# Kernel optimization log

Measured on AMD Instinct MI355X. Metric: run time of the kernel, lower is better.

Reference implementation:

```python
import jax, jax.numpy as jnp
import numpy as np
import math

N, S, R = 1, 128, 256
CM, CZ, C, MSA_H, PAIR_H, CTM, FF = 256, 128, 32, 8, 4, 128, 4
SCALE = 1.0 / math.sqrt(C)


def _ln(x, w, b):
    m = jnp.mean(x, -1, keepdims=True)
    v = jnp.var(x, -1, keepdims=True)
    return (x - m) / jnp.sqrt(v + 1e-5) * w + b


def _gated_attn(x, gate_w, qkv_w, out_w, head, bias=None):
    # x: [n, s, r, cin]; attention over r within each (n, s, head)
    n, s, r, _ = x.shape
    gate = jax.nn.sigmoid(x @ gate_w).reshape(n, s, r, head, C)
    qkv = (x @ qkv_w).reshape(n, s, r, 3, head, C)
    q, k, v = qkv[..., 0, :, :], qkv[..., 1, :, :], qkv[..., 2, :, :]
    sim = jax.nn.softmax(jnp.einsum('nsqhc,nskhc->nshqk', q, k) * SCALE, axis=-1)
    if bias is not None:
        sim = sim + bias  # NOTE: source adds bias AFTER softmax; kept faithful
    att = jnp.einsum('nshqk,nskhc->nsqhc', sim, v) * gate
    return att.reshape(n, s, r, head * C) @ out_w


def _tri_mul(x, n1w, n1b, n2w, n2b, p1, p2, p3, p4, p5, p6, incoming):
    xn = _ln(x, n1w, n1b)
    a = jax.nn.sigmoid(xn @ p1) * (xn @ p2)
    b = jax.nn.sigmoid(xn @ p3) * (xn @ p4)
    if incoming:
        p = jnp.einsum('nrsk,nrtk->nstk', a, b)
        g = jnp.swapaxes(jax.nn.sigmoid(xn @ p6), 1, 2)
    else:
        p = jnp.einsum('nsrk,ntrk->nstk', a, b)
        g = jax.nn.sigmoid(xn @ p6)
    return (_ln(p, n2w, n2b) @ p5) * g


def setup_inputs() -> dict:
    keys = iter(jax.random.split(jax.random.key(0), 80))

    def rn(shape, scale=0.02):
        return jax.random.normal(next(keys), shape, dtype=jnp.float32) * scale

    ones = lambda n: jnp.ones((n,), jnp.float32)
    zeros = lambda n: jnp.zeros((n,), jnp.float32)
    d = dict(
        msa_repr=rn((N, S, R, CM), 1.0),
        pair_repr=rn((N, R, R, CZ), 1.0),
        row_norm_m_w=ones(CM), row_norm_m_b=zeros(CM),
        row_norm_z_w=ones(CZ), row_norm_z_b=zeros(CZ),
        row_gate=rn((CM, MSA_H * C)), row_qkv=rn((CM, 3 * MSA_H * C)),
        row_out=rn((MSA_H * C, CM)), row_bias=rn((CZ, MSA_H)),
        col_norm_w=ones(CM), col_norm_b=zeros(CM),
        col_gate=rn((CM, MSA_H * C)), col_qkv=rn((CM, 3 * MSA_H * C)),
        col_out=rn((MSA_H * C, CM)),
        mt_norm_w=ones(CM), mt_norm_b=zeros(CM),
        mt_p1=rn((CM, FF * CM)), mt_p2=rn((FF * CM, CM)),
        outer_norm_w=ones(CM), outer_norm_b=zeros(CM),
        outer_p1=rn((CM, C)), outer_p2=rn((CM, C)), outer_out=rn((C * C, CZ)),
        tmo_n1_w=ones(CZ), tmo_n1_b=zeros(CZ), tmo_n2_w=ones(CTM), tmo_n2_b=zeros(CTM),
        tmo_p1=rn((CZ, CTM)), tmo_p2=rn((CZ, CTM)), tmo_p3=rn((CZ, CTM)), tmo_p4=rn((CZ, CTM)),
        tmo_p5=rn((CTM, CZ)), tmo_p6=rn((CZ, CZ)),
        tmi_n1_w=ones(CZ), tmi_n1_b=zeros(CZ), tmi_n2_w=ones(CTM), tmi_n2_b=zeros(CTM),
        tmi_p1=rn((CZ, CTM)), tmi_p2=rn((CZ, CTM)), tmi_p3=rn((CZ, CTM)), tmi_p4=rn((CZ, CTM)),
        tmi_p5=rn((CTM, CZ)), tmi_p6=rn((CZ, CZ)),
        tas_norm_w=ones(CZ), tas_norm_b=zeros(CZ),
        tas_gate=rn((CZ, PAIR_H * C)), tas_qkv=rn((CZ, 3 * PAIR_H * C)),
        tas_out=rn((PAIR_H * C, CZ)), tas_bias=rn((CZ, PAIR_H)),
        tae_norm_w=ones(CZ), tae_norm_b=zeros(CZ),
        tae_gate=rn((CZ, PAIR_H * C)), tae_qkv=rn((CZ, 3 * PAIR_H * C)),
        tae_out=rn((PAIR_H * C, CZ)), tae_bias=rn((CZ, PAIR_H)),
        pt_norm_w=ones(CZ), pt_norm_b=zeros(CZ),
        pt_p1=rn((CZ, FF * CZ)), pt_p2=rn((FF * CZ, CZ)),
    )
    return d


def reference(msa_repr, pair_repr, row_norm_m_w, row_norm_m_b, row_norm_z_w, row_norm_z_b, row_gate, row_qkv, row_out, row_bias, col_norm_w, col_norm_b, col_gate, col_qkv, col_out, mt_norm_w, mt_norm_b, mt_p1, mt_p2, outer_norm_w, outer_norm_b, outer_p1, outer_p2, outer_out, tmo_n1_w, tmo_n1_b, tmo_n2_w, tmo_n2_b, tmo_p1, tmo_p2, tmo_p3, tmo_p4, tmo_p5, tmo_p6, tmi_n1_w, tmi_n1_b, tmi_n2_w, tmi_n2_b, tmi_p1, tmi_p2, tmi_p3, tmi_p4, tmi_p5, tmi_p6, tas_norm_w, tas_norm_b, tas_gate, tas_qkv, tas_out, tas_bias, tae_norm_w, tae_norm_b, tae_gate, tae_qkv, tae_out, tae_bias, pt_norm_w, pt_norm_b, pt_p1, pt_p2):
    msa, pair = msa_repr, pair_repr
    # 1. MSA row attention with pair bias
    xm = _ln(msa, row_norm_m_w, row_norm_m_b)
    xz = _ln(pair, row_norm_z_w, row_norm_z_b)
    bias = jnp.transpose(xz @ row_bias, (0, 3, 1, 2))[:, None]  # [N,1,H,R,R]
    msa = msa + _gated_attn(xm, row_gate, row_qkv, row_out, MSA_H, bias)
    # 2. MSA column attention
    xm = _ln(msa, col_norm_w, col_norm_b)
    msa = msa + jnp.swapaxes(_gated_attn(jnp.swapaxes(xm, 1, 2), col_gate, col_qkv, col_out, MSA_H), 1, 2)
    # 3. MSA transition
    xm = _ln(msa, mt_norm_w, mt_norm_b)
    msa = msa + jax.nn.relu(xm @ mt_p1) @ mt_p2
    # 4. outer product mean (no division in source; sum over s)
    xm = _ln(msa, outer_norm_w, outer_norm_b)
    a = jnp.swapaxes(xm @ outer_p1, 1, 2)  # [n,r,s,c]
    b = jnp.swapaxes(xm @ outer_p2, 1, 2)  # [n,t,s,c]
    outer = jnp.einsum('nrsc,ntse->nrtce', a, b).reshape(a.shape[0], a.shape[1], b.shape[1], C * C)
    pair = pair + outer @ outer_out
    # 5/6. triangle multiplicative updates (outgoing then incoming)
    pair = pair + _tri_mul(pair, tmo_n1_w, tmo_n1_b, tmo_n2_w, tmo_n2_b, tmo_p1, tmo_p2, tmo_p3, tmo_p4, tmo_p5, tmo_p6, False)
    pair = pair + _tri_mul(pair, tmi_n1_w, tmi_n1_b, tmi_n2_w, tmi_n2_b, tmi_p1, tmi_p2, tmi_p3, tmi_p4, tmi_p5, tmi_p6, True)
    # 7. triangle attention (node start)
    xz = _ln(pair, tas_norm_w, tas_norm_b)
    bias = jnp.transpose(xz @ tas_bias, (0, 1, 3, 2))[:, :, :, None, :]  # [N,S,H,1,R]
    pair = pair + _gated_attn(xz, tas_gate, tas_qkv, tas_out, PAIR_H, bias)
    # 8. triangle attention (node end): transpose residue axes
    xz = jnp.swapaxes(_ln(pair, tae_norm_w, tae_norm_b), 1, 2)
    bias = jnp.transpose(xz @ tae_bias, (0, 1, 3, 2))[:, :, :, None, :]
    pair = pair + jnp.swapaxes(_gated_attn(xz, tae_gate, tae_qkv, tae_out, PAIR_H, bias), 1, 2)
    # 9. pair transition
    xz = _ln(pair, pt_norm_w, pt_norm_b)
    pair = pair + jax.nn.relu(xz @ pt_p1) @ pt_p2
    return msa, pair
```

## Files before the change

kernel.cpp:

```cpp
#include <hip/hip_runtime.h>
#include <hip/hip_bf16.h>
#include <stdint.h>

typedef __hip_bfloat16 bf16;
typedef __attribute__((ext_vector_type(4))) int   i32x4;
typedef __attribute__((ext_vector_type(4))) float f32x4;


__device__ __forceinline__ float toF(float x){ return x; }
__device__ __forceinline__ float toF(bf16 x){ return __bfloat162float(x); }
__device__ __forceinline__ bf16  toB(float x){ return __float2bfloat16(x); }

__device__ __forceinline__ void gload16(const bf16* g, bf16* l){
    __builtin_amdgcn_global_load_lds((const __attribute__((address_space(1))) void*)g,
                                     (__attribute__((address_space(3))) void*)l, 16, 0, 0);
}

__global__ void cvt_w_k(const void* __restrict__ in, bf16* __restrict__ out, int n,
                        const uint32_t* __restrict__ probe){
    bool isbf = (probe[0] == 0x3F803F80u);
    int i = blockIdx.x*256 + threadIdx.x;
    if (i < n) out[i] = isbf ? ((const bf16*)in)[i] : toB(((const float*)in)[i]);
}
__global__ void cvt_wT_k(const void* __restrict__ in, bf16* __restrict__ out, int K, int N,
                         const uint32_t* __restrict__ probe){
    bool isbf = (probe[0] == 0x3F803F80u);
    int i = blockIdx.x*256 + threadIdx.x;
    if (i < K*N){
        float v = isbf ? toF(((const bf16*)in)[i]) : ((const float*)in)[i];
        int k = i / N, n = i - k*N;
        out[(size_t)n*K + k] = toB(v);
    }
}
__global__ void in2f_k(const void* __restrict__ in, float* __restrict__ out, int n,
                       const uint32_t* __restrict__ probe){
    bool isbf = (probe[0] == 0x3F803F80u);
    int i = blockIdx.x*256 + threadIdx.x;
    if (i < n) out[i] = isbf ? toF(((const bf16*)in)[i]) : ((const float*)in)[i];
}

template<typename T>
__global__ void ln_k(const T* __restrict__ x, const bf16* __restrict__ w, const bf16* __restrict__ b,
                     bf16* __restrict__ out, int D){
    int row = blockIdx.x, c = threadIdx.x;
    float v = toF(x[(size_t)row*D + c]);
    float s1 = v, s2 = v*v;
    #pragma unroll
    for (int o=32;o>0;o>>=1){ s1 += __shfl_down(s1,o); s2 += __shfl_down(s2,o); }
    __shared__ float r1[4], r2[4];
    int lane = c & 63, wid = c >> 6;
    if (lane==0){ r1[wid]=s1; r2[wid]=s2; }
    __syncthreads();
    int nw = blockDim.x >> 6;
    float m=0.f, q=0.f;
    for (int i=0;i<nw;i++){ m+=r1[i]; q+=r2[i]; }
    m /= (float)D; q = q/(float)D - m*m;
    float inv = rsqrtf(q + 1e-5f);
    out[(size_t)row*D + c] = toB((v-m)*inv*toF(w[c]) + toF(b[c]));
}

template<int MODE, int HN>
__global__ __launch_bounds__(256) void bproj_k(const bf16* __restrict__ xz, const bf16* __restrict__ Wb,
                                               float* __restrict__ outb){
    __shared__ float WbS[128*HN];
    const int i = blockIdx.x, t = threadIdx.x;
    for (int idx = t; idx < 128*HN; idx += 256) WbS[idx] = toF(Wb[idx]);
    __syncthreads();
    const bf16* row = xz + ((size_t)i*256 + t)*128;
    float d[HN] = {};
    #pragma unroll 4
    for (int c8 = 0; c8 < 16; ++c8){
        uint4 v = *(const uint4*)(row + c8*8);
        bf16 tmp[8]; *(uint4*)tmp = v;
        #pragma unroll
        for (int u=0;u<8;u++){
            float x = toF(tmp[u]);
            #pragma unroll
            for (int h=0;h<HN;h++) d[h] += x * WbS[(c8*8+u)*HN + h];
        }
    }
    #pragma unroll
    for (int h=0;h<HN;h++){
        size_t idx = (MODE==0) ? ((size_t)h*65536 + (size_t)i*256 + t)
                   : (MODE==1) ? ((size_t)(i*HN+h)*256 + t)
                               : ((size_t)(t*HN+h)*256 + i);
        outb[idx] = d[h];
    }
}

template<int ACT, int MUL, int RES>
__global__ __launch_bounds__(256) void mgemm_k(const bf16* __restrict__ A, const bf16* __restrict__ Bt,
                                               bf16* __restrict__ C, float* __restrict__ Res,
                                               const bf16* __restrict__ Mul,
                                               int M, int N, int K, int lda, int ldbt, int ldc,
                                               int res_off, int gtrans){
    __shared__ alignas(16) bf16 As[128*32];
    __shared__ alignas(16) bf16 Bs[128*32];
    const int tid  = threadIdx.x;
    const int m0   = blockIdx.y << 7, n0 = blockIdx.x << 7;
    const int lane = tid & 63, w = tid >> 6;
    const int wr   = (w >> 1) << 6, wc = (w & 1) << 6;
    const int fr   = lane & 15, fq = lane >> 4;
    const int sr = tid >> 2, sc = (tid & 3) << 3;
    const bf16* ga = A  + (size_t)(m0 + sr)*lda  + sc;
    const bf16* gb = Bt + (size_t)(n0 + sr)*ldbt + sc;
    bf16* la = As + tid*8;
    bf16* lb = Bs + tid*8;
    const size_t gaS = (size_t)64*lda, gbS = (size_t)64*ldbt;

    f32x4 acc[4][4] = {};
    for (int k0=0; k0<K; k0+=32){
        gload16(ga, la);        gload16(ga + gaS, la + 2048);
        gload16(gb, lb);        gload16(gb + gbS, lb + 2048);
        ga += 32; gb += 32;
        __syncthreads();
        i32x4 af[4], bv[4];
        #pragma unroll
        for (int i=0;i<4;i++) af[i] = *(const i32x4*)(As + ((wr + i*16 + fr) << 5) + (fq << 3));
        #pragma unroll
        for (int j=0;j<4;j++) bv[j] = *(const i32x4*)(Bs + ((wc + j*16 + fr) << 5) + (fq << 3));
        #pragma unroll
        for (int i=0;i<4;i++)
            #pragma unroll
            for (int j=0;j<4;j++)
                asm("v_mfma_f32_16x16x32_bf16 %0, %1, %2, %0"
                    : "+v"(acc[i][j]) : "v"(af[i]), "v"(bv[j]));
        __syncthreads();
    }
    #pragma unroll
    for (int i=0;i<4;i++){
        const int mB = m0 + wr + i*16 + (fq << 2);
        #pragma unroll
        for (int j=0;j<4;j++){
            const int n = n0 + wc + j*16 + fr;
            #pragma unroll
            for (int r=0;r<4;r++){
                int m = mB + r;
                float x = acc[i][j][r];
                if (ACT==1) x = 1.f/(1.f + __expf(-x));
                else if (ACT==2) x = fmaxf(x, 0.f);
                if (MUL){
                    int mr = gtrans ? (((m & 255) << 8) | (m >> 8)) : m;
                    x *= toF(Mul[(size_t)mr*N + n]);
                }
                if (RES) Res[(size_t)(m + res_off)*N + n] += x;
                else     C[(size_t)m*ldc + n] = toB(x);
            }
        }
    }
}

template<int ACT, int MUL, int RES, int GATE>
__global__ __launch_bounds__(256) void sgemm_k(const bf16* __restrict__ A,
        const bf16* __restrict__ Bt1, const bf16* __restrict__ Bt2,
        bf16* __restrict__ C, float* __restrict__ Res, const bf16* __restrict__ Mul,
        int M, int lda, int ldbt, int ldc, int ldmul, int res_off, int gtrans){
    __shared__ alignas(16) bf16 Bs1[128*128];
    __shared__ alignas(16) bf16 Bs2[GATE ? 128*128 : 16];
    const int tid = threadIdx.x;
    for (int idx = tid; idx < 2048; idx += 256){
        int n = idx >> 4, cc = idx & 15;
        int sc = (cc ^ (n & 15)) << 3;
        *(uint4*)(Bs1 + n*128 + sc) = *(const uint4*)(Bt1 + (size_t)n*ldbt + (cc<<3));
        if (GATE)
            *(uint4*)(Bs2 + n*128 + sc) = *(const uint4*)(Bt2 + (size_t)n*ldbt + (cc<<3));
    }
    __syncthreads();
    const int lane = tid & 63, w = tid >> 6;
    const int fr = lane & 15, fq = lane >> 4;
    const int mb = blockIdx.x*128 + w*32;
    f32x4 acc[2][8] = {};
    f32x4 acc2[2][8] = {};
    #pragma unroll
    for (int k0=0;k0<4;k0++){
        i32x4 af[2];
        #pragma unroll
        for (int i=0;i<2;i++)
            af[i] = *(const i32x4*)(A + (size_t)(mb + i*16 + fr)*lda + k0*32 + fq*8);
        const int co = ((k0*4 + fq) ^ fr) << 3;
        #pragma unroll
        for (int j=0;j<8;j++){
            i32x4 bf1 = *(const i32x4*)(Bs1 + (j*16+fr)*128 + co);
            #pragma unroll
            for (int i=0;i<2;i++)
                asm("v_mfma_f32_16x16x32_bf16 %0, %1, %2, %0"
                    : "+v"(acc[i][j]) : "v"(af[i]), "v"(bf1));
            if (GATE){
                i32x4 bf2 = *(const i32x4*)(Bs2 + (j*16+fr)*128 + co);
                #pragma unroll
                for (int i=0;i<2;i++)
                    asm("v_mfma_f32_16x16x32_bf16 %0, %1, %2, %0"
                        : "+v"(acc2[i][j]) : "v"(af[i]), "v"(bf2));
            }
        }
    }
    #pragma unroll
    for (int i=0;i<2;i++){
        #pragma unroll
        for (int j=0;j<8;j++){
            const int n = j*16 + fr;
            #pragma unroll
            for (int r=0;r<4;r++){
                int m = mb + i*16 + (fq<<2) + r;
                float x = acc[i][j][r];
                if (GATE) x = acc2[i][j][r] / (1.f + __expf(-x));
                else if (ACT==1) x = 1.f/(1.f + __expf(-x));
                else if (ACT==2) x = fmaxf(x, 0.f);
                if (MUL){
                    int mr = gtrans ? (((m & 255) << 8) | (m >> 8)) : m;
                    x *= toF(Mul[(size_t)mr*ldmul + n]);
                }
                if (RES) Res[(size_t)(m + res_off)*128 + n] += x;
                else     C[(size_t)m*ldc + n] = toB(x);
            }
        }
    }
}

__global__ __launch_bounds__(256) void btrimul_k(const bf16* __restrict__ aT, const bf16* __restrict__ bT,
                                                 bf16* __restrict__ pT){
    __shared__ alignas(16) bf16 As[128*32];
    __shared__ alignas(16) bf16 Bs[128*32];
    const int tid  = threadIdx.x;
    const int m0   = blockIdx.y << 7, n0 = blockIdx.x << 7;
    const size_t zb = (size_t)blockIdx.z << 16;
    const int lane = tid & 63, w = tid >> 6;
    const int wr   = (w >> 1) << 6, wc = (w & 1) << 6;
    const int fr   = lane & 15, fq = lane >> 4;
    const int sr = tid >> 2, sc = (tid & 3) << 3;
    const bf16* ga = aT + zb + (size_t)(m0 + sr)*256 + sc;
    const bf16* gb = bT + zb + (size_t)(n0 + sr)*256 + sc;
    bf16* la = As + tid*8;
    bf16* lb = Bs + tid*8;
    const size_t gS = (size_t)64*256;

    f32x4 acc[4][4] = {};
    for (int k0=0; k0<256; k0+=32){
        gload16(ga, la);        gload16(ga + gS, la + 2048);
        gload16(gb, lb);        gload16(gb + gS, lb + 2048);
        ga += 32; gb += 32;
        __syncthreads();
        i32x4 af[4], bv[4];
        #pragma unroll
        for (int i=0;i<4;i++) af[i] = *(const i32x4*)(As + ((wr + i*16 + fr) << 5) + (fq << 3));
        #pragma unroll
        for (int j=0;j<4;j++) bv[j] = *(const i32x4*)(Bs + ((wc + j*16 + fr) << 5) + (fq << 3));
        #pragma unroll
        for (int i=0;i<4;i++)
            #pragma unroll
            for (int j=0;j<4;j++)
                asm("v_mfma_f32_16x16x32_bf16 %0, %1, %2, %0"
                    : "+v"(acc[i][j]) : "v"(af[i]), "v"(bv[j]));
        __syncthreads();
    }
    #pragma unroll
    for (int i=0;i<4;i++){
        const int mB = m0 + wr + i*16 + (fq << 2);
        #pragma unroll
        for (int j=0;j<4;j++){
            const int n = n0 + wc + j*16 + fr;
            #pragma unroll
            for (int r=0;r<4;r++)
                pT[zb + (size_t)(mB + r)*256 + n] = toB(acc[i][j][r]);
        }
    }
}

__global__ __launch_bounds__(256) void rc2k_k(const bf16* __restrict__ in, bf16* __restrict__ out, int swap){
    __shared__ uint16_t T[128][137];
    const int tt = blockIdx.x, tid = threadIdx.x;
    size_t base_pp, out_off; int ppstride;
    if (!swap){ base_pp = (size_t)tt*128;                  ppstride = 1;   out_off = (size_t)tt*128; }
    else      { int J = tt>>1, I0 = (tt&1)*128;
                base_pp = (size_t)I0*256 + J;              ppstride = 256; out_off = (size_t)J*256 + I0; }
    for (int it=0; it<8; ++it){
        int idx = tid + it*256;
        int r = idx >> 4, c8 = (idx & 15) << 3;
        uint4 v = *(const uint4*)(in + (base_pp + (size_t)r*ppstride)*128 + c8);
        uint16_t tmp[8]; *(uint4*)tmp = v;
        #pragma unroll
        for (int t=0;t<8;t++) T[r][c8+t] = tmp[t];
    }
    __syncthreads();
    for (int it=0; it<8; ++it){
        int idx = tid + it*256;
        int k = idx >> 4, r8 = (idx & 15) << 3;
        uint16_t tmp[8];
        #pragma unroll
        for (int t=0;t<8;t++) tmp[t] = T[r8+t][k];
        *(uint4*)(out + (size_t)k*65536 + out_off + r8) = *(uint4*)tmp;
    }
}
__global__ __launch_bounds__(256) void k2rc_k(const bf16* __restrict__ in, bf16* __restrict__ out){
    __shared__ uint16_t T[128][137];
    const int tt = blockIdx.x, tid = threadIdx.x;
    const size_t a0 = (size_t)tt*128;
    for (int it=0; it<8; ++it){
        int idx = tid + it*256;
        int k = idx >> 4, r8 = (idx & 15) << 3;
        uint4 v = *(const uint4*)(in + (size_t)k*65536 + a0 + r8);
        uint16_t tmp[8]; *(uint4*)tmp = v;
        #pragma unroll
        for (int t=0;t<8;t++) T[r8+t][k] = tmp[t];
    }
    __syncthreads();
    for (int it=0; it<8; ++it){
        int idx = tid + it*256;
        int r = idx >> 4, c8 = (idx & 15) << 3;
        uint16_t tmp[8];
        #pragma unroll
        for (int t=0;t<8;t++) tmp[t] = T[r][c8+t];
        *(uint4*)(out + (a0 + r)*128 + c8) = *(uint4*)tmp;
    }
}

template<int ACT, int MUL, int RES>
__global__ __launch_bounds__(256) void gemm_k(const bf16* __restrict__ A, const bf16* __restrict__ Bw,
                                              bf16* __restrict__ C, float* __restrict__ Res,
                                              const bf16* __restrict__ Mul,
                                              int M, int N, int K, int ldb, int res_off, int gtrans){
    __shared__ float As[64][33];
    __shared__ float Bs[32][65];
    int tid = threadIdx.x;
    int m0 = blockIdx.y*64, n0 = blockIdx.x*64;
    int tx = tid & 15, ty = tid >> 4;
    float acc[4][4] = {};
    for (int k0=0; k0<K; k0+=32){
        for (int i=tid; i<64*32; i+=256){
            int r = i>>5, cc = i&31;
            As[r][cc] = toF(A[(size_t)(m0+r)*K + k0 + cc]);
        }
        for (int i=tid; i<32*64; i+=256){
            int r = i>>6, cc = i&63; int col = n0+cc;
            Bs[r][cc] = (col < N) ? toF(Bw[(size_t)(k0+r)*ldb + col]) : 0.f;
        }
        __syncthreads();
        #pragma unroll 8
        for (int k=0;k<32;k++){
            float a4[4], b4[4];
            #pragma unroll
            for (int i=0;i<4;i++) a4[i] = As[ty*4+i][k];
            #pragma unroll
            for (int j=0;j<4;j++) b4[j] = Bs[k][tx*4+j];
            #pragma unroll
            for (int i=0;i<4;i++)
                #pragma unroll
                for (int j=0;j<4;j++) acc[i][j] += a4[i]*b4[j];
        }
        __syncthreads();
    }
    #pragma unroll
    for (int i=0;i<4;i++){
        int m = m0 + ty*4 + i;
        #pragma unroll
        for (int j=0;j<4;j++){
            int n = n0 + tx*4 + j;
            if (n >= N) continue;
            float x = acc[i][j];
            if (ACT==1) x = 1.f/(1.f + __expf(-x));
            else if (ACT==2) x = fmaxf(x, 0.f);
            if (MUL){
                int mr = gtrans ? (((m & 255) << 8) | (m >> 8)) : m;
                x *= toF(Mul[(size_t)mr*N + n]);
            }
            if (RES) Res[(size_t)(m + res_off)*N + n] += x;
            else     C[(size_t)m*N + n] = toB(x);
        }
    }
}

template<int BIAS, int L>
__global__ __launch_bounds__(256) void attn4_k(bf16* __restrict__ QO,
                                               const bf16* __restrict__ Kp, const bf16* __restrict__ Vp,
                                               const float* __restrict__ bias,
                                               int H, int GN, int sO, int sL){
    constexpr int MW  = L/4;
    constexpr int IFR = MW/16;
    constexpr int KC  = 32;
    constexpr int NCH = L/KC;
    constexpr int VP  = L + 8;
    __shared__ alignas(16) bf16 K_lds[L*40];
    __shared__ alignas(16) bf16 VT_lds[32*VP];
    __shared__ alignas(16) bf16 P_lds[L*40];
    __shared__ float red[8*32 + 32];
    const int o = blockIdx.y, h = blockIdx.x, tid = threadIdx.x;
    const int lane = tid & 63, w = tid >> 6;
    const int fr = lane & 15, fq = lane >> 4;

    for (int idx = tid; idx < L*4; idx += 256){
        int l = idx >> 2, c8 = (idx & 3) << 3;
        size_t p = (size_t)(o*sO + l*sL)*GN + h*32 + c8;
        *(uint4*)(K_lds + l*40 + c8) = *(const uint4*)(Kp + p);
        uint4 vv = *(const uint4*)(Vp + p);
        bf16 tmp[8]; *(uint4*)tmp = vv;
        #pragma unroll
        for (int t=0;t<8;t++) VT_lds[(c8+t)*VP + l] = tmp[t];
    }
    __syncthreads();

    float* ObS = red + 256;
    if (BIAS == 2){
        int c = tid & 31, g = tid >> 5;
        const float* bp = bias + (size_t)(o*H + h)*256;
        float p = 0.f;
        for (int k = g*(L/8); k < (g+1)*(L/8); ++k)
            p += bp[k] * toF(VT_lds[c*VP + k]);
        red[g*32 + c] = p;
        __syncthreads();
        if (tid < 32){
            float s = 0.f;
            #pragma unroll
            for (int g2=0; g2<8; ++g2) s += red[g2*32 + tid];
            ObS[tid] = s;
        }
        __syncthreads();
    }

    i32x4 qf[IFR];
    #pragma unroll
    for (int i=0;i<IFR;i++){
        int q = w*MW + i*16 + fr;
        qf[i] = *(const i32x4*)(QO + (size_t)(o*sO + q*sL)*GN + h*32 + fq*8);
    }
    bf16* Pw = P_lds + w*MW*40;
    f32x4 accO[IFR][2] = {};
    f32x4 accB[IFR][2] = {};
    float lsum[IFR][4] = {};

    for (int ch=0; ch<NCH; ++ch){
        const int k0 = ch*KC;
        f32x4 sa[IFR][2] = {};
        i32x4 kf[2];
        #pragma unroll
        for (int j=0;j<2;j++) kf[j] = *(const i32x4*)(K_lds + (k0 + j*16 + fr)*40 + fq*8);
        #pragma unroll
        for (int i=0;i<IFR;i++)
            #pragma unroll
            for (int j=0;j<2;j++)
                asm("v_mfma_f32_16x16x32_bf16 %0, %1, %2, %0"
                    : "+v"(sa[i][j]) : "v"(qf[i]), "v"(kf[j]));
        #pragma unroll
        for (int i=0;i<IFR;i++)
            #pragma unroll
            for (int j=0;j<2;j++)
                #pragma unroll
                for (int r=0;r<4;r++){
                    float e = __expf(sa[i][j][r] * 0.17677669529663687f);
                    lsum[i][r] += e;
                    Pw[(i*16 + fq*4 + r)*40 + j*16 + fr] = toB(e);
                }
        i32x4 vf[2];
        #pragma unroll
        for (int j=0;j<2;j++) vf[j] = *(const i32x4*)(VT_lds + (j*16 + fr)*VP + k0 + fq*8);
        #pragma unroll
        for (int i=0;i<IFR;i++){
            i32x4 pa = *(const i32x4*)(Pw + (i*16 + fr)*40 + fq*8);
            #pragma unroll
            for (int j=0;j<2;j++)
                asm("v_mfma_f32_16x16x32_bf16 %0, %1, %2, %0"
                    : "+v"(accO[i][j]) : "v"(pa), "v"(vf[j]));
        }
        if (BIAS == 1){
            #pragma unroll
            for (int it=0; it<32; ++it){
                int q = it*2 + (lane>>5), kk = lane&31;
                Pw[q*40 + kk] = toB(bias[(size_t)h*65536 + (size_t)(w*MW + q)*256 + k0 + kk]);
            }
            #pragma unroll
            for (int i=0;i<IFR;i++){
                i32x4 pa = *(const i32x4*)(Pw + (i*16 + fr)*40 + fq*8);
                #pragma unroll
                for (int j=0;j<2;j++)
                    asm("v_mfma_f32_16x16x32_bf16 %0, %1, %2, %0"
                        : "+v"(accB[i][j]) : "v"(pa), "v"(vf[j]));
            }
        }
    }
    #pragma unroll
    for (int i=0;i<IFR;i++)
        #pragma unroll
        for (int r=0;r<4;r++){
            float s = lsum[i][r];
            s += __shfl_xor(s, 1); s += __shfl_xor(s, 2);
            s += __shfl_xor(s, 4); s += __shfl_xor(s, 8);
            lsum[i][r] = 1.f / s;
        }
    #pragma unroll
    for (int i=0;i<IFR;i++)
        #pragma unroll
        for (int j=0;j<2;j++)
            #pragma unroll
            for (int r=0;r<4;r++){
                int q = w*MW + i*16 + fq*4 + r;
                int c = j*16 + fr;
                float v = accO[i][j][r]*lsum[i][r];
                if (BIAS==1) v += accB[i][j][r];
                if (BIAS==2) v += ObS[c];
                QO[(size_t)(o*sO + q*sL)*GN + h*32 + c] = toB(v);
            }
}

__global__ void mulsig2_k(bf16* __restrict__ a, int n){
    int i = blockIdx.x*256 + threadIdx.x;
    if (i < n){
        int m = i >> 8, c = i & 255;
        size_t o = (size_t)m*768 + c;
        float sg = 1.f/(1.f + __expf(-toF(a[o + 256])));
        a[o] = toB(toF(a[o]) * sg);
    }
}

__global__ __launch_bounds__(256) void outer_k(const bf16* __restrict__ ap, const bf16* __restrict__ bp,
                                               bf16* __restrict__ outc, int r0){
    int t = blockIdx.x, rl = blockIdx.y, r = r0 + rl;
    __shared__ float As[128*32], Bs[128*32];
    for (int idx=threadIdx.x; idx<128*32; idx+=256){
        int s = idx>>5, c = idx&31;
        As[idx] = toF(ap[((size_t)s*256 + r)*32 + c]);
        Bs[idx] = toF(bp[((size_t)s*256 + t)*32 + c]);
    }
    __syncthreads();
    int ce0 = threadIdx.x*4;
    int c = ce0 >> 5, e0 = ce0 & 31;
    float acc[4] = {0.f,0.f,0.f,0.f};
    for (int s=0;s<128;s++){
        float av = As[s*32 + c];
        #pragma unroll
        for (int j=0;j<4;j++) acc[j] += av*Bs[s*32 + e0 + j];
    }
    size_t row = (size_t)rl*256 + t;
    #pragma unroll
    for (int j=0;j<4;j++) outc[row*1024 + ce0 + j] = toB(acc[j]);
}

static bool tshape(int i, int& K, int& N){
    switch(i){
        case 6: case 8: case 12: case 14: K=256; N=256;  return true;
        case 7: case 13:                  K=256; N=768;  return true;
        case 17:                          K=256; N=1024; return true;
        case 18:                          K=1024;N=256;  return true;
        case 23:                          K=1024;N=128;  return true;
        case 47: case 53:                 K=128; N=384;  return true;
        case 58:                          K=128; N=512;  return true;
        case 59:                          K=512; N=128;  return true;
        default:
            if ((i>=28&&i<=33)||(i>=38&&i<=43)||i==46||i==48||i==52||i==54){ K=128; N=128; return true; }
            return false;
    }
}

extern "C" void kernel_launch(void* const* d_in, const int* in_sizes, int n_in,
                              void* d_out, int out_size, void* d_ws, size_t ws_size,
                              hipStream_t stream){
    (void)n_in; (void)out_size; (void)ws_size;
    const int MSA_N  = 128*256*256;
    const int PAIR_N = 256*256*128;
    const uint32_t* probe = (const uint32_t*)d_in[2];

    char*  w     = (char*)d_ws;
    bf16*  wsts  = (bf16*)(w);
    float* biasF = (float*)(w + 4194304);
    bf16*  lnb   = (bf16*)(w + 6291456);
    bf16*  bufA  = (bf16*)(w + 23068672);
    bf16*  bufB  = (bf16*)(w + 39845888);
    bf16*  bufC  = (bf16*)(w + 56623104);

    float* msaF  = (float*)d_out;
    float* pairF = msaF + MSA_N;

    size_t woff[64]; { size_t acc = 0;
        for (int i=2;i<60;i++){ woff[i] = acc; acc += ((size_t)in_sizes[i] + 63) & ~(size_t)63; } }
    #define W(i) (wsts + woff[i])
    for (int i=2;i<60;i++){
        int tk, tn;
        if (tshape(i, tk, tn))
            cvt_wT_k<<<(in_sizes[i]+255)/256,256,0,stream>>>(d_in[i], W(i), tk, tn, probe);
        else
            cvt_w_k<<<(in_sizes[i]+255)/256,256,0,stream>>>(d_in[i], W(i), in_sizes[i], probe);
    }

    in2f_k<<<32768,256,0,stream>>>(d_in[0], msaF,  MSA_N,  probe);
    in2f_k<<<32768,256,0,stream>>>(d_in[1], pairF, PAIR_N, probe);

    ln_k<float><<<32768,256,0,stream>>>(msaF, W(2), W(3), lnb, 256);
    ln_k<float><<<65536,128,0,stream>>>(pairF, W(4), W(5), bufC, 128);
    bproj_k<0,8><<<256,256,0,stream>>>(bufC, W(9), biasF);
    mgemm_k<0,0,0><<<dim3(6,256),256,0,stream>>>(lnb, W(7), bufA, nullptr, nullptr,
                                                 32768,768,256, 256,256,768, 0,0);
    attn4_k<1,256><<<dim3(8,128),256,0,stream>>>(bufA, bufA+256, bufA+512, biasF, 8, 768, 256, 1);
    mgemm_k<0,0,0><<<dim3(2,256),256,0,stream>>>(lnb, W(6), bufA+256, nullptr, nullptr,
                                                 32768,256,256, 256,256,768, 0,0);
    mulsig2_k<<<32768,256,0,stream>>>(bufA, MSA_N);
    mgemm_k<0,0,1><<<dim3(2,256),256,0,stream>>>(bufA, W(8), nullptr, msaF, nullptr,
                                                 32768,256,256, 768,256,256, 0,0);

    ln_k<float><<<32768,256,0,stream>>>(msaF, W(10), W(11), lnb, 256);
    mgemm_k<0,0,0><<<dim3(6,256),256,0,stream>>>(lnb, W(13), bufA, nullptr, nullptr,
                                                 32768,768,256, 256,256,768, 0,0);
    attn4_k<0,128><<<dim3(8,256),256,0,stream>>>(bufA, bufA+256, bufA+512, nullptr, 8, 768, 1, 256);
    mgemm_k<0,0,0><<<dim3(2,256),256,0,stream>>>(lnb, W(12), bufA+256, nullptr, nullptr,
                                                 32768,256,256, 256,256,768, 0,0);
    mulsig2_k<<<32768,256,0,stream>>>(bufA, MSA_N);
    mgemm_k<0,0,1><<<dim3(2,256),256,0,stream>>>(bufA, W(14), nullptr, msaF, nullptr,
                                                 32768,256,256, 768,256,256, 0,0);

    ln_k<float><<<32768,256,0,stream>>>(msaF, W(15), W(16), lnb, 256);
    for (int ch=0; ch<4; ++ch){
        mgemm_k<2,0,0><<<dim3(2,256),256,0,stream>>>(lnb, W(17)+ch*65536, bufA, nullptr, nullptr,
                                                     32768,256,256, 256,256,256, 0,0);
        mgemm_k<0,0,1><<<dim3(2,256),256,0,stream>>>(bufA, W(18)+ch*256, nullptr, msaF, nullptr,
                                                     32768,256,256, 256,1024,256, 0,0);
    }

    ln_k<float><<<32768,256,0,stream>>>(msaF, W(19), W(20), lnb, 256);
    gemm_k<0,0,0><<<dim3(1,512),256,0,stream>>>(lnb, W(21), bufA, nullptr, nullptr, 32768,32,256, 32, 0,0);
    gemm_k<0,0,0><<<dim3(1,512),256,0,stream>>>(lnb, W(22), bufB, nullptr, nullptr, 32768,32,256, 32, 0,0);
    for (int ch=0; ch<8; ++ch){
        outer_k<<<dim3(256,32),256,0,stream>>>(bufA, bufB, lnb, ch*32);
        mgemm_k<0,0,1><<<dim3(1,64),256,0,stream>>>(lnb, W(23), nullptr, pairF, nullptr,
                                                    8192,128,1024, 1024,1024,128, ch*8192,0);
    }

    for (int tm=0; tm<2; ++tm){
        int o = tm ? 34 : 24;
        int inc = tm;
        ln_k<float><<<65536,128,0,stream>>>(pairF, W(o+0), W(o+1), lnb, 128);
        sgemm_k<0,0,0,1><<<512,256,0,stream>>>(lnb, W(o+4), W(o+5), bufA, nullptr, nullptr,
                                               65536, 128,128,128,0, 0,0);
        sgemm_k<0,0,0,1><<<512,256,0,stream>>>(lnb, W(o+6), W(o+7), bufB, nullptr, nullptr,
                                               65536, 128,128,128,0, 0,0);
        rc2k_k<<<512,256,0,stream>>>(bufA, bufC, inc);
        rc2k_k<<<512,256,0,stream>>>(bufB, bufA, inc);
        btrimul_k<<<dim3(2,2,128),256,0,stream>>>(bufC, bufA, bufB);
        k2rc_k<<<512,256,0,stream>>>(bufB, bufC);
        ln_k<bf16><<<65536,128,0,stream>>>(bufC, W(o+2), W(o+3), bufC, 128);
        sgemm_k<1,0,0,0><<<512,256,0,stream>>>(lnb, W(o+9), nullptr, bufA, nullptr, nullptr,
                                               65536, 128,128,128,0, 0,0);
        sgemm_k<0,1,1,0><<<512,256,0,stream>>>(bufC, W(o+8), nullptr, nullptr, pairF, bufA,
                                               65536, 128,128,0,128, 0, inc);
    }

    ln_k<float><<<65536,128,0,stream>>>(pairF, W(44), W(45), lnb, 128);
    bproj_k<1,4><<<256,256,0,stream>>>(lnb, W(49), biasF);
    mgemm_k<0,0,0><<<dim3(3,512),256,0,stream>>>(lnb, W(47), bufA, nullptr, nullptr,
                                                 65536,384,128, 128,128,384, 0,0);
    attn4_k<2,256><<<dim3(4,256),256,0,stream>>>(bufA, bufA+128, bufA+256, biasF, 4, 384, 256, 1);
    sgemm_k<1,1,0,0><<<512,256,0,stream>>>(lnb, W(46), nullptr, bufA+128, nullptr, bufA,
                                           65536, 128,128,384,384, 0,0);
    sgemm_k<0,0,1,0><<<512,256,0,stream>>>(bufA+128, W(48), nullptr, nullptr, pairF, nullptr,
                                           65536, 384,128,0,0, 0,0);
    ln_k<float><<<65536,128,0,stream>>>(pairF, W(50), W(51), lnb, 128);
    bproj_k<2,4><<<256,256,0,stream>>>(lnb, W(55), biasF);
    mgemm_k<0,0,0><<<dim3(3,512),256,0,stream>>>(lnb, W(53), bufA, nullptr, nullptr,
                                                 65536,384,128, 128,128,384, 0,0);
    attn4_k<2,256><<<dim3(4,256),256,0,stream>>>(bufA, bufA+128, bufA+256, biasF, 4, 384, 1, 256);
    sgemm_k<1,1,0,0><<<512,256,0,stream>>>(lnb, W(52), nullptr, bufA+128, nullptr, bufA,
                                           65536, 128,128,384,384, 0,0);
    sgemm_k<0,0,1,0><<<512,256,0,stream>>>(bufA+128, W(54), nullptr, nullptr, pairF, nullptr,
                                           65536, 384,128,0,0, 0,0);

    ln_k<float><<<65536,128,0,stream>>>(pairF, W(56), W(57), lnb, 128);
    for (int ch=0; ch<4; ++ch){
        sgemm_k<2,0,0,0><<<512,256,0,stream>>>(lnb, W(58)+ch*16384, nullptr, bufA, nullptr, nullptr,
                                               65536, 128,128,128,0, 0,0);
        sgemm_k<0,0,1,0><<<512,256,0,stream>>>(bufA, W(59)+ch*128, nullptr, nullptr, pairF, nullptr,
                                               65536, 128,512,0,0, 0,0);
    }
}
```

Baseline: 2.557 ms.

## Batch weight conversions into one launch and read attention K fragments directly from global

The 58 per-weight conversion kernel launches become a single launch that indexes each weight by blockIdx.y and uses grid-stride loops, which cuts launch overhead. Separately, the attention kernel stops staging K in LDS and loads each MFMA K fragment straight from global memory. This saves LDS space and a copy, but the K loads become strided global reads inside the inner loop, which adds latency.

```diff
diff --git a/kernel.cpp b/kernel.cpp
--- a/kernel.cpp
+++ b/kernel.cpp
@@ -16,20 +16,24 @@
                                      (__attribute__((address_space(3))) void*)l, 16, 0, 0);
 }
 
-__global__ void cvt_w_k(const void* __restrict__ in, bf16* __restrict__ out, int n,
-                        const uint32_t* __restrict__ probe){
+#define NW_IN 58
+struct WStage {
+    const void* src[NW_IN];
+    int off[NW_IN];
+    int K[NW_IN], N[NW_IN];
+};
+__global__ __launch_bounds__(256) void cvt_all_k(WStage t, bf16* __restrict__ base,
+                                                 const uint32_t* __restrict__ probe){
     bool isbf = (probe[0] == 0x3F803F80u);
-    int i = blockIdx.x*256 + threadIdx.x;
-    if (i < n) out[i] = isbf ? ((const bf16*)in)[i] : toB(((const float*)in)[i]);
-}
-__global__ void cvt_wT_k(const void* __restrict__ in, bf16* __restrict__ out, int K, int N,
-                         const uint32_t* __restrict__ probe){
-    bool isbf = (probe[0] == 0x3F803F80u);
-    int i = blockIdx.x*256 + threadIdx.x;
-    if (i < K*N){
+    const int wi = blockIdx.y;
+    const void* in = t.src[wi];
+    bf16* out = base + t.off[wi];
+    const int K = t.K[wi], N = t.N[wi];
+    const int total = K ? K*N : N;
+    for (int i = blockIdx.x*256 + threadIdx.x; i < total; i += gridDim.x*256){
         float v = isbf ? toF(((const bf16*)in)[i]) : ((const float*)in)[i];
-        int k = i / N, n = i - k*N;
-        out[(size_t)n*K + k] = toB(v);
+        if (K){ int k = i / N, n = i - k*N; out[(size_t)n*K + k] = toB(v); }
+        else    out[i] = toB(v);
     }
 }
 __global__ void in2f_k(const void* __restrict__ in, float* __restrict__ out, int n,
@@ -379,7 +383,6 @@
     constexpr int KC  = 32;
     constexpr int NCH = L/KC;
     constexpr int VP  = L + 8;
-    __shared__ alignas(16) bf16 K_lds[L*40];
     __shared__ alignas(16) bf16 VT_lds[32*VP];
     __shared__ alignas(16) bf16 P_lds[L*40];
     __shared__ float red[8*32 + 32];
@@ -390,7 +393,6 @@
     for (int idx = tid; idx < L*4; idx += 256){
         int l = idx >> 2, c8 = (idx & 3) << 3;
         size_t p = (size_t)(o*sO + l*sL)*GN + h*32 + c8;
-        *(uint4*)(K_lds + l*40 + c8) = *(const uint4*)(Kp + p);
         uint4 vv = *(const uint4*)(Vp + p);
         bf16 tmp[8]; *(uint4*)tmp = vv;
         #pragma unroll
@@ -422,6 +424,9 @@
         int q = w*MW + i*16 + fr;
         qf[i] = *(const i32x4*)(QO + (size_t)(o*sO + q*sL)*GN + h*32 + fq*8);
     }
+    const bf16* kbase = Kp + (size_t)o*sO*GN + h*32 + fq*8 + (size_t)fr*sL*GN;
+    const size_t kstep = (size_t)sL*GN;
+
     bf16* Pw = P_lds + w*MW*40;
     f32x4 accO[IFR][2] = {};
     f32x4 accB[IFR][2] = {};
@@ -432,7 +437,7 @@
         f32x4 sa[IFR][2] = {};
         i32x4 kf[2];
         #pragma unroll
-        for (int j=0;j<2;j++) kf[j] = *(const i32x4*)(K_lds + (k0 + j*16 + fr)*40 + fq*8);
+        for (int j=0;j<2;j++) kf[j] = *(const i32x4*)(kbase + (size_t)(k0 + j*16)*kstep);
         #pragma unroll
         for (int i=0;i<IFR;i++)
             #pragma unroll
@@ -571,12 +576,17 @@
     size_t woff[64]; { size_t acc = 0;
         for (int i=2;i<60;i++){ woff[i] = acc; acc += ((size_t)in_sizes[i] + 63) & ~(size_t)63; } }
     #define W(i) (wsts + woff[i])
-    for (int i=2;i<60;i++){
-        int tk, tn;
-        if (tshape(i, tk, tn))
-            cvt_wT_k<<<(in_sizes[i]+255)/256,256,0,stream>>>(d_in[i], W(i), tk, tn, probe);
-        else
-            cvt_w_k<<<(in_sizes[i]+255)/256,256,0,stream>>>(d_in[i], W(i), in_sizes[i], probe);
+
+    {
+        WStage st;
+        for (int i=2;i<60;i++){
+            int tk, tn;
+            st.src[i-2] = d_in[i];
+            st.off[i-2] = (int)woff[i];
+            if (tshape(i, tk, tn)){ st.K[i-2]=tk; st.N[i-2]=tn; }
+            else                   { st.K[i-2]=0;  st.N[i-2]=in_sizes[i]; }
+        }
+        cvt_all_k<<<dim3(64, NW_IN),256,0,stream>>>(st, wsts, probe);
     }
 
     in2f_k<<<32768,256,0,stream>>>(d_in[0], msaF,  MSA_N,  probe);
```

After: 2.499 ms. 2.3% less time.
